# Kernel tuning notes

Measured on AMD Instinct MI355X. Metric: run time of the kernel, lower is better.

Reference implementation:

```python
import jax, jax.numpy as jnp
from jax import lax
import numpy as np
import math

DIM = 96      # channels
HEADS = 3     # num_heads
WS = 8        # window size
SHIFT = 4     # window_size // 2 (depth is odd -> shifted)
TLC = 64      # tlc_kernel
H = 264
W = 264


def _grid_idxes(h, w, k1, k2):
    # Faithful replication of the torch grids() tiling index logic (static ints).
    num_row = (h - 1) // k1 + 1
    num_col = (w - 1) // k2 + 1
    step_j = k2 if num_col == 1 else math.ceil((w - k2) / (num_col - 1) - 1e-8)
    step_i = k1 if num_row == 1 else math.ceil((h - k1) / (num_row - 1) - 1e-8)
    idxes = []
    i = 0
    last_i = False
    while i < h and not last_i:
        j = 0
        if i + k1 >= h:
            i = h - k1
            last_i = True
        last_j = False
        while j < w and not last_j:
            if j + k2 >= w:
                j = w - k2
                last_j = True
            idxes.append((i, j))
            j = j + step_j
        i = i + step_i
    return idxes


def setup_inputs() -> dict:
    key = jax.random.key(0)
    ks = jax.random.split(key, 4)
    return {
        "x": jax.random.normal(ks[0], (1, DIM, H, W), jnp.float32),
        "temperature": jnp.ones((HEADS, 1, 1), jnp.float32),
        "qkv_w": jax.random.normal(ks[1], (3 * DIM, DIM), jnp.float32) * 0.05,
        "dw_w": jax.random.normal(ks[2], (3 * DIM, 1, 3, 3), jnp.float32) * 0.1,
        "proj_w": jax.random.normal(ks[3], (DIM, DIM), jnp.float32) * 0.05,
    }


def reference(x, temperature, qkv_w, dw_w, proj_w):
    b, c, h, w = x.shape
    # depth % 2 == 1 -> cyclic shift
    x = jnp.roll(x, (-SHIFT, -SHIFT), axis=(2, 3))
    # 1x1 pointwise conv (no bias)
    qkv = jnp.einsum('oc,bchw->bohw', qkv_w, x)
    # 3x3 depthwise conv, padding 1
    qkv = lax.conv_general_dilated(
        qkv, dw_w, window_strides=(1, 1), padding=[(1, 1), (1, 1)],
        feature_group_count=3 * c, dimension_numbers=('NCHW', 'OIHW', 'NCHW'))
    # --- TLC grids: overlapping tiles (eval path, b == 1) ---
    k1, k2 = min(h, TLC), min(w, TLC)
    idxes = _grid_idxes(h, w, k1, k2)
    parts = jnp.concatenate([qkv[:, :, i:i + k1, j:j + k2] for (i, j) in idxes], axis=0)  # [T,3c,k1,k2]
    T, C3, th, tw = parts.shape
    nh, nw = th // WS, tw // WS
    # window partition: b c (h b0) (w b1) -> (b h w) c b0 b1 -> flatten spatial
    win = parts.reshape(T, C3, nh, WS, nw, WS).transpose(0, 2, 4, 1, 3, 5)
    win = win.reshape(T * nh * nw, C3, WS * WS)  # [Bw, 3c, 64]
    q, k, v = jnp.split(win, 3, axis=1)  # each [Bw, c, 64]
    ch = c // HEADS
    q = q.reshape(-1, HEADS, ch, WS * WS)
    k = k.reshape(-1, HEADS, ch, WS * WS)
    v = v.reshape(-1, HEADS, ch, WS * WS)
    # L2 normalize along token dim (F.normalize eps=1e-12)
    q = q / jnp.maximum(jnp.linalg.norm(q, axis=-1, keepdims=True), 1e-12)
    k = k / jnp.maximum(jnp.linalg.norm(k, axis=-1, keepdims=True), 1e-12)
    # channel attention: [Bw, head, ch, ch]
    attn = jax.nn.relu(jnp.einsum('bhcn,bhdn->bhcd', q, k) * temperature)
    out = jnp.einsum('bhcd,bhdn->bhcn', attn, v)  # [Bw, head, ch, 64]
    out = out.reshape(-1, c, WS, WS)
    # window merge back to tiles
    out = out.reshape(T, nh, nw, c, WS, WS).transpose(0, 3, 1, 4, 2, 5).reshape(T, c, th, tw)
    # --- TLC grids_inverse: scatter-add overlapping tiles and average ---
    preds = jnp.zeros((b, c, h, w), x.dtype)
    cnt = np.zeros((h, w), np.float32)
    for t, (i, j) in enumerate(idxes):
        preds = preds.at[0, :, i:i + k1, j:j + k2].add(out[t])
        cnt[i:i + k1, j:j + k2] += 1.0
    preds = preds / jnp.asarray(cnt)
    # 1x1 output projection
    out = jnp.einsum('oc,bchw->bohw', proj_w, preds)
    # undo cyclic shift
    return jnp.roll(out, (SHIFT, SHIFT), axis=(2, 3))
```

## Files before the change

kernel.cpp:

```cpp
#include <hip/hip_runtime.h>
#include <hip/hip_bf16.h>

#define HW_ 69696
#define W_ 264
#define H_ 264

typedef short bf16x8 __attribute__((ext_vector_type(8)));
typedef float f32x4 __attribute__((ext_vector_type(4)));

static __device__ __forceinline__ unsigned short f2b(float f) {
  __hip_bfloat16 h = __float2bfloat16(f);
  return *reinterpret_cast<unsigned short*>(&h);
}
static __device__ __forceinline__ float b2f(unsigned short u) {
  __hip_bfloat16 h;
  *reinterpret_cast<unsigned short*>(&h) = u;
  return __bfloat162float(h);
}
static __device__ __forceinline__ float lo_f(unsigned int u) {
  union { unsigned int i; float f; } c; c.i = u << 16; return c.f;
}
static __device__ __forceinline__ float hi_f(unsigned int u) {
  union { unsigned int i; float f; } c; c.i = u & 0xffff0000u; return c.f;
}

__global__ __launch_bounds__(256, 4) void k_gemm(const float* __restrict__ x,
                                                 const float* __restrict__ w,
                                                 unsigned short* __restrict__ outb) {
  __shared__ __align__(16) char smem[19968];
  unsigned short* As = (unsigned short*)smem;
  unsigned short* Cs = (unsigned short*)smem;

  const int tid = threadIdx.x;
  const int wid = tid >> 6, lane = tid & 63;
  const int quad = lane >> 4, lo = lane & 15;
  const int px0 = blockIdx.x * 64;
  const int px = px0 + wid * 16 + lo;

  const int y = px / W_, xx = px - y * W_;
  int y2 = y + 4; if (y2 >= H_) y2 -= H_;
  int x2 = xx + 4; if (x2 >= W_) x2 -= W_;
  const float* xb = x + y2 * W_ + x2;

  bf16x8 bf[3];
#pragma unroll
  for (int ks = 0; ks < 3; ++ks) {
    const float* xp = xb + (size_t)(ks * 32 + quad * 8) * HW_;
    float f[8];
#pragma unroll
    for (int i = 0; i < 8; ++i) f[i] = xp[(size_t)i * HW_];
    union { bf16x8 v; unsigned short s[8]; } u;
#pragma unroll
    for (int i = 0; i < 8; ++i) u.s[i] = f2b(f[i]);
    bf[ks] = u.v;
  }

  for (int oc = 0; oc < 3; ++oc) {
    __syncthreads();
    const float* wp = w + oc * 96 * 96;
    for (int l = tid; l < 96 * 24; l += 256) {
      int o = l / 24, c4 = (l - (l / 24) * 24) * 4;
      float4 v = *(const float4*)&wp[o * 96 + c4];
      unsigned int p0 = (unsigned int)f2b(v.x) | ((unsigned int)f2b(v.y) << 16);
      unsigned int p1 = (unsigned int)f2b(v.z) | ((unsigned int)f2b(v.w) << 16);
      *(uint2*)&As[o * 104 + c4] = make_uint2(p0, p1);
    }
    __syncthreads();

    f32x4 acc[6];
#pragma unroll
    for (int mt = 0; mt < 6; ++mt) acc[mt] = {0.f, 0.f, 0.f, 0.f};
#pragma unroll
    for (int ks = 0; ks < 3; ++ks) {
      const int kb = ks * 32 + quad * 8;
#pragma unroll
      for (int mt = 0; mt < 6; ++mt) {
        bf16x8 a = *(const bf16x8*)&As[(mt * 16 + lo) * 104 + kb];
        acc[mt] = __builtin_amdgcn_mfma_f32_16x16x32_bf16(a, bf[ks], acc[mt], 0, 0, 0);
      }
    }
    __syncthreads();

    const int pxl = wid * 16 + lo;
#pragma unroll
    for (int mt = 0; mt < 6; ++mt) {
      unsigned int p0 = (unsigned int)f2b(acc[mt][0]) | ((unsigned int)f2b(acc[mt][1]) << 16);
      unsigned int p1 = (unsigned int)f2b(acc[mt][2]) | ((unsigned int)f2b(acc[mt][3]) << 16);
      *(uint2*)&Cs[pxl * 104 + mt * 16 + quad * 4] = make_uint2(p0, p1);
    }
    __syncthreads();

    for (int i = tid; i < 64 * 12; i += 256) {
      int pxl2 = i & 63, j = i >> 6;
      *((uint4*)outb + (size_t)(oc * 12 + j) * HW_ + px0 + pxl2) =
          ((const uint4*)(Cs + pxl2 * 104))[j];
    }
  }
}

__global__ __launch_bounds__(256) void k_dw(const unsigned short* __restrict__ qkv,
                                            const float* __restrict__ dw,
                                            unsigned short* __restrict__ out) {
  __shared__ __align__(16) uint4 inS[18 * 66];
  const int tid = threadIdx.x;
  const int x0 = blockIdx.x * 64;
  const int y0 = blockIdx.y * 16;
  const int u = blockIdx.z;
  const uint4* plane = (const uint4*)qkv + (size_t)u * HW_;
  const float* wp = dw + u * 72;
  float wv[72];
#pragma unroll
  for (int i = 0; i < 72; ++i) wv[i] = wp[i];

  for (int idx = tid; idx < 18 * 66; idx += 256) {
    int rr = idx / 66, cc = idx - rr * 66;
    int gy = y0 - 1 + rr, gx = x0 - 1 + cc;
    uint4 v = make_uint4(0u, 0u, 0u, 0u);
    if ((unsigned)gy < (unsigned)H_ && (unsigned)gx < (unsigned)W_)
      v = plane[gy * W_ + gx];
    inS[idx] = v;
  }
  __syncthreads();

#pragma unroll
  for (int k = 0; k < 4; ++k) {
    const int oidx = k * 256 + tid;
    const int ro = oidx >> 6, co = oidx & 63;
    const int y = y0 + ro, x = x0 + co;
    float acc[8] = {0.f, 0.f, 0.f, 0.f, 0.f, 0.f, 0.f, 0.f};
#pragma unroll
    for (int dy = 0; dy < 3; ++dy)
#pragma unroll
      for (int dx = 0; dx < 3; ++dx) {
        uint4 v = inS[(ro + dy) * 66 + co + dx];
        float w0 = wv[0 * 9 + dy * 3 + dx], w1 = wv[1 * 9 + dy * 3 + dx];
        float w2 = wv[2 * 9 + dy * 3 + dx], w3 = wv[3 * 9 + dy * 3 + dx];
        float w4 = wv[4 * 9 + dy * 3 + dx], w5 = wv[5 * 9 + dy * 3 + dx];
        float w6 = wv[6 * 9 + dy * 3 + dx], w7 = wv[7 * 9 + dy * 3 + dx];
        acc[0] += w0 * lo_f(v.x); acc[1] += w1 * hi_f(v.x);
        acc[2] += w2 * lo_f(v.y); acc[3] += w3 * hi_f(v.y);
        acc[4] += w4 * lo_f(v.z); acc[5] += w5 * hi_f(v.z);
        acc[6] += w6 * lo_f(v.w); acc[7] += w7 * hi_f(v.w);
      }
    if (y < H_ && x < W_) {
      uint4 o;
      o.x = (unsigned int)f2b(acc[0]) | ((unsigned int)f2b(acc[1]) << 16);
      o.y = (unsigned int)f2b(acc[2]) | ((unsigned int)f2b(acc[3]) << 16);
      o.z = (unsigned int)f2b(acc[4]) | ((unsigned int)f2b(acc[5]) << 16);
      o.w = (unsigned int)f2b(acc[6]) | ((unsigned int)f2b(acc[7]) << 16);
      *((uint4*)out + (size_t)u * HW_ + y * W_ + x) = o;
    }
  }
}

#define P1 200
#define P8 1608
__global__ __launch_bounds__(192) void k_attn(const unsigned short* __restrict__ qd,
                                              const float* __restrict__ temp,
                                              unsigned short* __restrict__ tout) {
  __shared__ __align__(16) unsigned short flat[8 * P8];
  __shared__ __align__(16) unsigned short attnL[3 * 32 * 40];
  __shared__ float invn[3 * 32];
  const int tid = threadIdx.x;
  const int wi = blockIdx.x, t = blockIdx.y;
  const int i0 = (t / 5) * 50, j0 = (t % 5) * 50;
  const int wy = wi >> 3, wx = wi & 7;
  const int gy0 = i0 + wy * 8, gx0 = j0 + wx * 8;

  {
    const size_t base = (size_t)gy0 * W_ + gx0;
    for (int idx = tid; idx < 24 * 64; idx += 192) {
      int u = idx >> 6, rj = idx & 63, r = rj >> 3, j = rj & 7;
      uint4 v = ((const uint4*)qd)[(size_t)u * HW_ + base + r * W_ + j];
      ((uint4*)flat)[r * 201 + j * 25 + u] = v;
    }
  }
  __syncthreads();

  const int h = tid >> 6, lane = tid & 63;
  const int quad = lane >> 4, lo = lane & 15;
  const int cb = h * 32;

  bf16x8 qf[2][2], kf[2][2];
#pragma unroll
  for (int mt = 0; mt < 2; ++mt)
#pragma unroll
    for (int kt = 0; kt < 2; ++kt) {
      const int rbase = (kt * 4 + quad) * P8;
      const int cq = cb + mt * 16 + lo;
      const int ck = 96 + cb + mt * 16 + lo;
      bf16x8 q8, k8;
#pragma unroll
      for (int j = 0; j < 8; ++j) {
        q8[j] = (short)flat[rbase + j * P1 + cq];
        k8[j] = (short)flat[rbase + j * P1 + ck];
      }
      qf[mt][kt] = q8;
      kf[mt][kt] = k8;
    }

  f32x4 S[2][2];
#pragma unroll
  for (int mt = 0; mt < 2; ++mt)
#pragma unroll
    for (int nt = 0; nt < 2; ++nt) {
      S[mt][nt] = {0.f, 0.f, 0.f, 0.f};
#pragma unroll
      for (int kt = 0; kt < 2; ++kt)
        S[mt][nt] = __builtin_amdgcn_mfma_f32_16x16x32_bf16(qf[mt][kt], kf[nt][kt], S[mt][nt], 0, 0, 0);
    }

  float ivk[2];
#pragma unroll
  for (int mt = 0; mt < 2; ++mt) {
    float sq = 0.f, sk = 0.f;
#pragma unroll
    for (int kt = 0; kt < 2; ++kt)
#pragma unroll
      for (int j = 0; j < 8; ++j) {
        float a = b2f((unsigned short)qf[mt][kt][j]);
        float b = b2f((unsigned short)kf[mt][kt][j]);
        sq += a * a;
        sk += b * b;
      }
    sq += __shfl_xor(sq, 16);
    sq += __shfl_xor(sq, 32);
    sk += __shfl_xor(sk, 16);
    sk += __shfl_xor(sk, 32);
    if (quad == 0) invn[h * 32 + mt * 16 + lo] = 1.f / fmaxf(sqrtf(sq), 1e-12f);
    ivk[mt] = 1.f / fmaxf(sqrtf(sk), 1e-12f);
  }
  __syncthreads();

  const float ts = temp[h];
#pragma unroll
  for (int mt = 0; mt < 2; ++mt)
#pragma unroll
    for (int nt = 0; nt < 2; ++nt)
#pragma unroll
      for (int r = 0; r < 4; ++r) {
        int c = mt * 16 + quad * 4 + r;
        float v = S[mt][nt][r] * invn[h * 32 + c] * ivk[nt] * ts;
        attnL[(h * 32 + c) * 40 + nt * 16 + lo] = f2b(fmaxf(v, 0.f));
      }
  __syncthreads();

  bf16x8 af[2];
#pragma unroll
  for (int mt = 0; mt < 2; ++mt)
    af[mt] = *(const bf16x8*)&attnL[(h * 32 + mt * 16 + lo) * 40 + quad * 8];

  const int uv = 24 + h * 4 + quad;
  f32x4 O[2][4];
#pragma unroll
  for (int nt = 0; nt < 4; ++nt) {
    const int px = nt * 16 + lo;
    const size_t gpx = (size_t)(gy0 + (px >> 3)) * W_ + gx0 + (px & 7);
    uint4 vraw = ((const uint4*)qd)[(size_t)uv * HW_ + gpx];
    bf16x8 vf = *reinterpret_cast<bf16x8*>(&vraw);
#pragma unroll
    for (int mt = 0; mt < 2; ++mt) {
      f32x4 z = {0.f, 0.f, 0.f, 0.f};
      O[mt][nt] = __builtin_amdgcn_mfma_f32_16x16x32_bf16(af[mt], vf, z, 0, 0, 0);
    }
  }
  __syncthreads();

  unsigned short* Cs = flat;
#pragma unroll
  for (int mt = 0; mt < 2; ++mt)
#pragma unroll
    for (int nt = 0; nt < 4; ++nt) {
      const int px = nt * 16 + lo;
      unsigned int p0 = (unsigned int)f2b(O[mt][nt][0]) | ((unsigned int)f2b(O[mt][nt][1]) << 16);
      unsigned int p1 = (unsigned int)f2b(O[mt][nt][2]) | ((unsigned int)f2b(O[mt][nt][3]) << 16);
      *(uint2*)&Cs[px * 104 + cb + mt * 16 + quad * 4] = make_uint2(p0, p1);
    }
  __syncthreads();

  for (int idx = tid; idx < 64 * 12; idx += 192) {
    int rec = idx / 12, u = idx - (idx / 12) * 12;
    int r = rec >> 3, j = rec & 7;
    size_t g = (size_t)t * 4096 + (wy * 8 + r) * 64 + wx * 8 + j;
    ((uint4*)tout)[g * 12 + u] = ((const uint4*)(Cs + rec * 104))[u];
  }
}

__global__ __launch_bounds__(256, 4) void k_avgproj(const float* __restrict__ w,
                                                    const unsigned short* __restrict__ tout,
                                                    float* __restrict__ outf) {
  __shared__ __align__(16) unsigned short As[96 * 104];
  const int tid = threadIdx.x;
  const int wid = tid >> 6, lane = tid & 63;
  const int quad = lane >> 4, lo = lane & 15;
  const int px0 = blockIdx.x * 64;
  const int px = px0 + wid * 16 + lo;

  for (int l = tid; l < 96 * 24; l += 256) {
    int o = l / 24, c4 = (l - (l / 24) * 24) * 4;
    float4 v = *(const float4*)&w[o * 96 + c4];
    unsigned int p0 = (unsigned int)f2b(v.x) | ((unsigned int)f2b(v.y) << 16);
    unsigned int p1 = (unsigned int)f2b(v.z) | ((unsigned int)f2b(v.w) << 16);
    *(uint2*)&As[o * 104 + c4] = make_uint2(p0, p1);
  }

  const int y = px / W_, xx = px - y * W_;
  int loy = (y >= 64) ? (y - 14) / 50 : 0;
  int hiy = y / 50; if (hiy > 4) hiy = 4;
  int lox = (xx >= 64) ? (xx - 14) / 50 : 0;
  int hix = xx / 50; if (hix > 4) hix = 4;
  float a24[24];
#pragma unroll
  for (int i = 0; i < 24; ++i) a24[i] = 0.f;
  int cnt = 0;
  for (int ty = loy; ty <= hiy; ++ty)
    for (int tx = lox; tx <= hix; ++tx) {
      size_t rec = (size_t)(ty * 5 + tx) * 4096 + ((y - ty * 50) << 6) + (xx - tx * 50);
      const uint4* rp = (const uint4*)tout + rec * 12 + quad;
#pragma unroll
      for (int ks = 0; ks < 3; ++ks) {
        uint4 v = rp[ks * 4];
        a24[ks * 8 + 0] += lo_f(v.x); a24[ks * 8 + 1] += hi_f(v.x);
        a24[ks * 8 + 2] += lo_f(v.y); a24[ks * 8 + 3] += hi_f(v.y);
        a24[ks * 8 + 4] += lo_f(v.z); a24[ks * 8 + 5] += hi_f(v.z);
        a24[ks * 8 + 6] += lo_f(v.w); a24[ks * 8 + 7] += hi_f(v.w);
      }
      ++cnt;
    }
  const float inv = 1.f / (float)cnt;
  bf16x8 bf[3];
#pragma unroll
  for (int ks = 0; ks < 3; ++ks) {
    union { bf16x8 v; unsigned short s[8]; } u;
#pragma unroll
    for (int i = 0; i < 8; ++i) u.s[i] = f2b(a24[ks * 8 + i] * inv);
    bf[ks] = u.v;
  }
  __syncthreads();

  f32x4 acc[6];
#pragma unroll
  for (int mt = 0; mt < 6; ++mt) acc[mt] = {0.f, 0.f, 0.f, 0.f};
#pragma unroll
  for (int ks = 0; ks < 3; ++ks) {
    const int kb = ks * 32 + quad * 8;
#pragma unroll
    for (int mt = 0; mt < 6; ++mt) {
      bf16x8 a = *(const bf16x8*)&As[(mt * 16 + lo) * 104 + kb];
      acc[mt] = __builtin_amdgcn_mfma_f32_16x16x32_bf16(a, bf[ks], acc[mt], 0, 0, 0);
    }
  }

  {
    int y2 = y + 4; if (y2 >= H_) y2 -= H_;
    int x2 = xx + 4; if (x2 >= W_) x2 -= W_;
    int tp = y2 * W_ + x2;
#pragma unroll
    for (int mt = 0; mt < 6; ++mt) {
      int row = mt * 16 + quad * 4;
#pragma unroll
      for (int r = 0; r < 4; ++r)
        outf[(size_t)(row + r) * HW_ + tp] = acc[mt][r];
    }
  }
}

extern "C" void kernel_launch(void* const* d_in, const int* in_sizes, int n_in,
                              void* d_out, int out_size, void* d_ws, size_t ws_size,
                              hipStream_t stream) {
  (void)in_sizes; (void)n_in; (void)out_size; (void)ws_size;
  const float* x = (const float*)d_in[0];
  const float* temp = (const float*)d_in[1];
  const float* qkvw = (const float*)d_in[2];
  const float* dww = (const float*)d_in[3];
  const float* projw = (const float*)d_in[4];
  float* out = (float*)d_out;

  char* ws = (char*)d_ws;
  const size_t SZQ = (size_t)288 * HW_ * 2;
  unsigned short* qkvb = (unsigned short*)ws;
  unsigned short* tout = (unsigned short*)ws;
  unsigned short* qkvd = (unsigned short*)(ws + SZQ);

  k_gemm<<<dim3(1089), 256, 0, stream>>>(x, qkvw, qkvb);
  k_dw<<<dim3(5, 17, 36), 256, 0, stream>>>(qkvb, dww, qkvd);
  k_attn<<<dim3(64, 25), 192, 0, stream>>>(qkvd, temp, tout);
  k_avgproj<<<dim3(1089), 256, 0, stream>>>(projw, tout, out);
}
```

Baseline: 150.1 us.

## Widen GEMM and depthwise tiles, run attention with 256-thread blocks

The QKV GEMM now handles 128 pixels per block with two N-tiles per wave, so each weight conversion into LDS is reused across twice as many pixels and the grid is roughly halved. The depthwise conv tile widens from 64 to 132 columns, which cuts halo overhead and the number of blocks. The attention kernel moves to 256 threads with a fourth wave that only helps with loads and stores, guarded by an active flag. The larger tiles raise register and LDS use per block, which may lower occupancy, and the extra attention wave sits idle during the compute phases.

```diff
diff --git a/kernel.cpp b/kernel.cpp
--- a/kernel.cpp
+++ b/kernel.cpp
@@ -27,32 +27,36 @@
 __global__ __launch_bounds__(256, 4) void k_gemm(const float* __restrict__ x,
                                                  const float* __restrict__ w,
                                                  unsigned short* __restrict__ outb) {
-  __shared__ __align__(16) char smem[19968];
+  __shared__ __align__(16) char smem[26624];
   unsigned short* As = (unsigned short*)smem;
   unsigned short* Cs = (unsigned short*)smem;
 
   const int tid = threadIdx.x;
   const int wid = tid >> 6, lane = tid & 63;
   const int quad = lane >> 4, lo = lane & 15;
-  const int px0 = blockIdx.x * 64;
-  const int px = px0 + wid * 16 + lo;
-
-  const int y = px / W_, xx = px - y * W_;
-  int y2 = y + 4; if (y2 >= H_) y2 -= H_;
-  int x2 = xx + 4; if (x2 >= W_) x2 -= W_;
-  const float* xb = x + y2 * W_ + x2;
-
-  bf16x8 bf[3];
-#pragma unroll
-  for (int ks = 0; ks < 3; ++ks) {
-    const float* xp = xb + (size_t)(ks * 32 + quad * 8) * HW_;
-    float f[8];
-#pragma unroll
-    for (int i = 0; i < 8; ++i) f[i] = xp[(size_t)i * HW_];
-    union { bf16x8 v; unsigned short s[8]; } u;
-#pragma unroll
-    for (int i = 0; i < 8; ++i) u.s[i] = f2b(f[i]);
-    bf[ks] = u.v;
+  const int px0 = blockIdx.x * 128;
+
+  bf16x8 bf[2][3];
+#pragma unroll
+  for (int nt = 0; nt < 2; ++nt) {
+    const int px = px0 + wid * 32 + nt * 16 + lo;
+    if (px < HW_) {
+      const int y = px / W_, xx = px - y * W_;
+      int y2 = y + 4; if (y2 >= H_) y2 -= H_;
+      int x2 = xx + 4; if (x2 >= W_) x2 -= W_;
+      const float* xb = x + y2 * W_ + x2;
+#pragma unroll
+      for (int ks = 0; ks < 3; ++ks) {
+        const float* xp = xb + (size_t)(ks * 32 + quad * 8) * HW_;
+        union { bf16x8 v; unsigned short s[8]; } u;
+#pragma unroll
+        for (int i = 0; i < 8; ++i) u.s[i] = f2b(xp[(size_t)i * HW_]);
+        bf[nt][ks] = u.v;
+      }
+    } else {
+#pragma unroll
+      for (int ks = 0; ks < 3; ++ks) bf[nt][ks] = bf16x8{0, 0, 0, 0, 0, 0, 0, 0};
+    }
   }
 
   for (int oc = 0; oc < 3; ++oc) {
@@ -67,33 +71,41 @@
     }
     __syncthreads();
 
-    f32x4 acc[6];
-#pragma unroll
-    for (int mt = 0; mt < 6; ++mt) acc[mt] = {0.f, 0.f, 0.f, 0.f};
+    f32x4 acc[6][2];
+#pragma unroll
+    for (int mt = 0; mt < 6; ++mt)
+#pragma unroll
+      for (int nt = 0; nt < 2; ++nt) acc[mt][nt] = {0.f, 0.f, 0.f, 0.f};
 #pragma unroll
     for (int ks = 0; ks < 3; ++ks) {
       const int kb = ks * 32 + quad * 8;
 #pragma unroll
       for (int mt = 0; mt < 6; ++mt) {
         bf16x8 a = *(const bf16x8*)&As[(mt * 16 + lo) * 104 + kb];
-        acc[mt] = __builtin_amdgcn_mfma_f32_16x16x32_bf16(a, bf[ks], acc[mt], 0, 0, 0);
+#pragma unroll
+        for (int nt = 0; nt < 2; ++nt)
+          acc[mt][nt] = __builtin_amdgcn_mfma_f32_16x16x32_bf16(a, bf[nt][ks], acc[mt][nt], 0, 0, 0);
       }
     }
     __syncthreads();
 
-    const int pxl = wid * 16 + lo;
-#pragma unroll
-    for (int mt = 0; mt < 6; ++mt) {
-      unsigned int p0 = (unsigned int)f2b(acc[mt][0]) | ((unsigned int)f2b(acc[mt][1]) << 16);
-      unsigned int p1 = (unsigned int)f2b(acc[mt][2]) | ((unsigned int)f2b(acc[mt][3]) << 16);
-      *(uint2*)&Cs[pxl * 104 + mt * 16 + quad * 4] = make_uint2(p0, p1);
+#pragma unroll
+    for (int nt = 0; nt < 2; ++nt) {
+      const int pxl = wid * 32 + nt * 16 + lo;
+#pragma unroll
+      for (int mt = 0; mt < 6; ++mt) {
+        unsigned int p0 = (unsigned int)f2b(acc[mt][nt][0]) | ((unsigned int)f2b(acc[mt][nt][1]) << 16);
+        unsigned int p1 = (unsigned int)f2b(acc[mt][nt][2]) | ((unsigned int)f2b(acc[mt][nt][3]) << 16);
+        *(uint2*)&Cs[pxl * 104 + mt * 16 + quad * 4] = make_uint2(p0, p1);
+      }
     }
     __syncthreads();
 
-    for (int i = tid; i < 64 * 12; i += 256) {
-      int pxl2 = i & 63, j = i >> 6;
-      *((uint4*)outb + (size_t)(oc * 12 + j) * HW_ + px0 + pxl2) =
-          ((const uint4*)(Cs + pxl2 * 104))[j];
+    for (int i = tid; i < 128 * 12; i += 256) {
+      int pxl = i & 127, j = i >> 7;
+      if (px0 + pxl < HW_)
+        *((uint4*)outb + (size_t)(oc * 12 + j) * HW_ + px0 + pxl) =
+            ((const uint4*)(Cs + pxl * 104))[j];
     }
   }
 }
@@ -101,9 +113,9 @@
 __global__ __launch_bounds__(256) void k_dw(const unsigned short* __restrict__ qkv,
                                             const float* __restrict__ dw,
                                             unsigned short* __restrict__ out) {
-  __shared__ __align__(16) uint4 inS[18 * 66];
+  __shared__ __align__(16) uint4 inS[18 * 134];
   const int tid = threadIdx.x;
-  const int x0 = blockIdx.x * 64;
+  const int x0 = blockIdx.x * 132;
   const int y0 = blockIdx.y * 16;
   const int u = blockIdx.z;
   const uint4* plane = (const uint4*)qkv + (size_t)u * HW_;
@@ -112,8 +124,8 @@
 #pragma unroll
   for (int i = 0; i < 72; ++i) wv[i] = wp[i];
 
-  for (int idx = tid; idx < 18 * 66; idx += 256) {
-    int rr = idx / 66, cc = idx - rr * 66;
+  for (int idx = tid; idx < 18 * 134; idx += 256) {
+    int rr = idx / 134, cc = idx - rr * 134;
     int gy = y0 - 1 + rr, gx = x0 - 1 + cc;
     uint4 v = make_uint4(0u, 0u, 0u, 0u);
     if ((unsigned)gy < (unsigned)H_ && (unsigned)gx < (unsigned)W_)
@@ -122,17 +134,17 @@
   }
   __syncthreads();
 
-#pragma unroll
-  for (int k = 0; k < 4; ++k) {
+  for (int k = 0; k < 9; ++k) {
     const int oidx = k * 256 + tid;
-    const int ro = oidx >> 6, co = oidx & 63;
+    if (oidx >= 16 * 132) break;
+    const int ro = oidx / 132, co = oidx - ro * 132;
     const int y = y0 + ro, x = x0 + co;
     float acc[8] = {0.f, 0.f, 0.f, 0.f, 0.f, 0.f, 0.f, 0.f};
 #pragma unroll
     for (int dy = 0; dy < 3; ++dy)
 #pragma unroll
       for (int dx = 0; dx < 3; ++dx) {
-        uint4 v = inS[(ro + dy) * 66 + co + dx];
+        uint4 v = inS[(ro + dy) * 134 + co + dx];
         float w0 = wv[0 * 9 + dy * 3 + dx], w1 = wv[1 * 9 + dy * 3 + dx];
         float w2 = wv[2 * 9 + dy * 3 + dx], w3 = wv[3 * 9 + dy * 3 + dx];
         float w4 = wv[4 * 9 + dy * 3 + dx], w5 = wv[5 * 9 + dy * 3 + dx];
@@ -142,7 +154,7 @@
         acc[4] += w4 * lo_f(v.z); acc[5] += w5 * hi_f(v.z);
         acc[6] += w6 * lo_f(v.w); acc[7] += w7 * hi_f(v.w);
       }
-    if (y < H_ && x < W_) {
+    if (y < H_) {
       uint4 o;
       o.x = (unsigned int)f2b(acc[0]) | ((unsigned int)f2b(acc[1]) << 16);
       o.y = (unsigned int)f2b(acc[2]) | ((unsigned int)f2b(acc[3]) << 16);
@@ -155,9 +167,9 @@
 
 #define P1 200
 #define P8 1608
-__global__ __launch_bounds__(192) void k_attn(const unsigned short* __restrict__ qd,
-                                              const float* __restrict__ temp,
-                                              unsigned short* __restrict__ tout) {
+__global__ __launch_bounds__(256, 4) void k_attn(const unsigned short* __restrict__ qd,
+                                                 const float* __restrict__ temp,
+                                                 unsigned short* __restrict__ tout) {
   __shared__ __align__(16) unsigned short flat[8 * P8];
   __shared__ __align__(16) unsigned short attnL[3 * 32 * 40];
   __shared__ float invn[3 * 32];
@@ -169,7 +181,7 @@
 
   {
     const size_t base = (size_t)gy0 * W_ + gx0;
-    for (int idx = tid; idx < 24 * 64; idx += 192) {
+    for (int idx = tid; idx < 24 * 64; idx += 256) {
       int u = idx >> 6, rj = idx & 63, r = rj >> 3, j = rj & 7;
       uint4 v = ((const uint4*)qd)[(size_t)u * HW_ + base + r * W_ + j];
       ((uint4*)flat)[r * 201 + j * 25 + u] = v;
@@ -180,105 +192,114 @@
   const int h = tid >> 6, lane = tid & 63;
   const int quad = lane >> 4, lo = lane & 15;
   const int cb = h * 32;
+  const bool act = (h < 3);
 
   bf16x8 qf[2][2], kf[2][2];
-#pragma unroll
-  for (int mt = 0; mt < 2; ++mt)
-#pragma unroll
-    for (int kt = 0; kt < 2; ++kt) {
-      const int rbase = (kt * 4 + quad) * P8;
-      const int cq = cb + mt * 16 + lo;
-      const int ck = 96 + cb + mt * 16 + lo;
-      bf16x8 q8, k8;
-#pragma unroll
-      for (int j = 0; j < 8; ++j) {
-        q8[j] = (short)flat[rbase + j * P1 + cq];
-        k8[j] = (short)flat[rbase + j * P1 + ck];
-      }
-      qf[mt][kt] = q8;
-      kf[mt][kt] = k8;
-    }
-
   f32x4 S[2][2];
-#pragma unroll
-  for (int mt = 0; mt < 2; ++mt)
-#pragma unroll
-    for (int nt = 0; nt < 2; ++nt) {
-      S[mt][nt] = {0.f, 0.f, 0.f, 0.f};
+  float ivk[2];
+  if (act) {
+#pragma unroll
+    for (int mt = 0; mt < 2; ++mt)
+#pragma unroll
+      for (int kt = 0; kt < 2; ++kt) {
+        const int rbase = (kt * 4 + quad) * P8;
+        const int cq = cb + mt * 16 + lo;
+        const int ck = 96 + cb + mt * 16 + lo;
+        bf16x8 q8, k8;
+#pragma unroll
+        for (int j = 0; j < 8; ++j) {
+          q8[j] = (short)flat[rbase + j * P1 + cq];
+          k8[j] = (short)flat[rbase + j * P1 + ck];
+        }
+        qf[mt][kt] = q8;
+        kf[mt][kt] = k8;
+      }
+
+#pragma unroll
+    for (int mt = 0; mt < 2; ++mt)
+#pragma unroll
+      for (int nt = 0; nt < 2; ++nt) {
+        S[mt][nt] = {0.f, 0.f, 0.f, 0.f};
+#pragma unroll
+        for (int kt = 0; kt < 2; ++kt)
+          S[mt][nt] = __builtin_amdgcn_mfma_f32_16x16x32_bf16(qf[mt][kt], kf[nt][kt], S[mt][nt], 0, 0, 0);
+      }
+
+#pragma unroll
+    for (int mt = 0; mt < 2; ++mt) {
+      float sq = 0.f, sk = 0.f;
 #pragma unroll
       for (int kt = 0; kt < 2; ++kt)
-        S[mt][nt] = __builtin_amdgcn_mfma_f32_16x16x32_bf16(qf[mt][kt], kf[nt][kt], S[mt][nt], 0, 0, 0);
-    }
-
-  float ivk[2];
-#pragma unroll
-  for (int mt = 0; mt < 2; ++mt) {
-    float sq = 0.f, sk = 0.f;
-#pragma unroll
-    for (int kt = 0; kt < 2; ++kt)
-#pragma unroll
-      for (int j = 0; j < 8; ++j) {
-        float a = b2f((unsigned short)qf[mt][kt][j]);
-        float b = b2f((unsigned short)kf[mt][kt][j]);
-        sq += a * a;
-        sk += b * b;
-      }
-    sq += __shfl_xor(sq, 16);
-    sq += __shfl_xor(sq, 32);
-    sk += __shfl_xor(sk, 16);
-    sk += __shfl_xor(sk, 32);
-    if (quad == 0) invn[h * 32 + mt * 16 + lo] = 1.f / fmaxf(sqrtf(sq), 1e-12f);
-    ivk[mt] = 1.f / fmaxf(sqrtf(sk), 1e-12f);
-  }
-  __syncthreads();
-
-  const float ts = temp[h];
-#pragma unroll
-  for (int mt = 0; mt < 2; ++mt)
-#pragma unroll
-    for (int nt = 0; nt < 2; ++nt)
-#pragma unroll
-      for (int r = 0; r < 4; ++r) {
-        int c = mt * 16 + quad * 4 + r;
-        float v = S[mt][nt][r] * invn[h * 32 + c] * ivk[nt] * ts;
-        attnL[(h * 32 + c) * 40 + nt * 16 + lo] = f2b(fmaxf(v, 0.f));
-      }
-  __syncthreads();
-
-  bf16x8 af[2];
-#pragma unroll
-  for (int mt = 0; mt < 2; ++mt)
-    af[mt] = *(const bf16x8*)&attnL[(h * 32 + mt * 16 + lo) * 40 + quad * 8];
-
-  const int uv = 24 + h * 4 + quad;
+#pragma unroll
+        for (int j = 0; j < 8; ++j) {
+          float a = b2f((unsigned short)qf[mt][kt][j]);
+          float b = b2f((unsigned short)kf[mt][kt][j]);
+          sq += a * a;
+          sk += b * b;
+        }
+      sq += __shfl_xor(sq, 16);
+      sq += __shfl_xor(sq, 32);
+      sk += __shfl_xor(sk, 16);
+      sk += __shfl_xor(sk, 32);
+      if (quad == 0) invn[h * 32 + mt * 16 + lo] = 1.f / fmaxf(sqrtf(sq), 1e-12f);
+      ivk[mt] = 1.f / fmaxf(sqrtf(sk), 1e-12f);
+    }
+  }
+  __syncthreads();
+
+  if (act) {
+    const float ts = temp[h];
+#pragma unroll
+    for (int mt = 0; mt < 2; ++mt)
+#pragma unroll
+      for (int nt = 0; nt < 2; ++nt)
+#pragma unroll
+        for (int r = 0; r < 4; ++r) {
+          int c = mt * 16 + quad * 4 + r;
+          float v = S[mt][nt][r] * invn[h * 32 + c] * ivk[nt] * ts;
+          attnL[(h * 32 + c) * 40 + nt * 16 + lo] = f2b(fmaxf(v, 0.f));
+        }
+  }
+  __syncthreads();
+
   f32x4 O[2][4];
-#pragma unroll
-  for (int nt = 0; nt < 4; ++nt) {
-    const int px = nt * 16 + lo;
-    const size_t gpx = (size_t)(gy0 + (px >> 3)) * W_ + gx0 + (px & 7);
-    uint4 vraw = ((const uint4*)qd)[(size_t)uv * HW_ + gpx];
-    bf16x8 vf = *reinterpret_cast<bf16x8*>(&vraw);
-#pragma unroll
-    for (int mt = 0; mt < 2; ++mt) {
-      f32x4 z = {0.f, 0.f, 0.f, 0.f};
-      O[mt][nt] = __builtin_amdgcn_mfma_f32_16x16x32_bf16(af[mt], vf, z, 0, 0, 0);
-    }
-  }
-  __syncthreads();
-
-  unsigned short* Cs = flat;
-#pragma unroll
-  for (int mt = 0; mt < 2; ++mt)
+  if (act) {
+    bf16x8 af[2];
+#pragma unroll
+    for (int mt = 0; mt < 2; ++mt)
+      af[mt] = *(const bf16x8*)&attnL[(h * 32 + mt * 16 + lo) * 40 + quad * 8];
+
+    const int uv = 24 + h * 4 + quad;
 #pragma unroll
     for (int nt = 0; nt < 4; ++nt) {
       const int px = nt * 16 + lo;
-      unsigned int p0 = (unsigned int)f2b(O[mt][nt][0]) | ((unsigned int)f2b(O[mt][nt][1]) << 16);
-      unsigned int p1 = (unsigned int)f2b(O[mt][nt][2]) | ((unsigned int)f2b(O[mt][nt][3]) << 16);
-      *(uint2*)&Cs[px * 104 + cb + mt * 16 + quad * 4] = make_uint2(p0, p1);
-    }
-  __syncthreads();
-
-  for (int idx = tid; idx < 64 * 12; idx += 192) {
+      const size_t gpx = (size_t)(gy0 + (px >> 3)) * W_ + gx0 + (px & 7);
+      uint4 vraw = ((const uint4*)qd)[(size_t)uv * HW_ + gpx];
+      bf16x8 vf = *reinterpret_cast<bf16x8*>(&vraw);
+#pragma unroll
+      for (int mt = 0; mt < 2; ++mt) {
+        f32x4 z = {0.f, 0.f, 0.f, 0.f};
+        O[mt][nt] = __builtin_amdgcn_mfma_f32_16x16x32_bf16(af[mt], vf, z, 0, 0, 0);
+      }
+    }
+  }
+  __syncthreads();
+
+  unsigned short* Cs = flat;
+  if (act) {
+#pragma unroll
+    for (int mt = 0; mt < 2; ++mt)
+#pragma unroll
+      for (int nt = 0; nt < 4; ++nt) {
+        const int px = nt * 16 + lo;
+        unsigned int p0 = (unsigned int)f2b(O[mt][nt][0]) | ((unsigned int)f2b(O[mt][nt][1]) << 16);
+        unsigned int p1 = (unsigned int)f2b(O[mt][nt][2]) | ((unsigned int)f2b(O[mt][nt][3]) << 16);
+        *(uint2*)&Cs[px * 104 + cb + mt * 16 + quad * 4] = make_uint2(p0, p1);
+      }
+  }
+  __syncthreads();
+
+  for (int idx = tid; idx < 64 * 12; idx += 256) {
     int rec = idx / 12, u = idx - (idx / 12) * 12;
     int r = rec >> 3, j = rec & 7;
     size_t g = (size_t)t * 4096 + (wy * 8 + r) * 64 + wx * 8 + j;
@@ -382,8 +403,8 @@
   unsigned short* tout = (unsigned short*)ws;
   unsigned short* qkvd = (unsigned short*)(ws + SZQ);
 
-  k_gemm<<<dim3(1089), 256, 0, stream>>>(x, qkvw, qkvb);
-  k_dw<<<dim3(5, 17, 36), 256, 0, stream>>>(qkvb, dww, qkvd);
-  k_attn<<<dim3(64, 25), 192, 0, stream>>>(qkvd, temp, tout);
+  k_gemm<<<dim3(545), 256, 0, stream>>>(x, qkvw, qkvb);
+  k_dw<<<dim3(2, 17, 36), 256, 0, stream>>>(qkvb, dww, qkvd);
+  k_attn<<<dim3(64, 25), 256, 0, stream>>>(qkvd, temp, tout);
   k_avgproj<<<dim3(1089), 256, 0, stream>>>(projw, tout, out);
 }
```

After: 151.8 us. About the same (+1.2%).

## Fuse pointwise qkv GEMM with depthwise 3x3 conv using halo tiles in LDS

Applied to the files above, without the earlier changes.

Merges the 1x1 qkv GEMM and the 3x3 depthwise conv into one kernel. Each block computes the GEMM on a 22x8 tile plus a one-pixel halo (24x10) and keeps the bf16 result in shared memory, then applies the depthwise conv directly from LDS. This removes the full round trip of the intermediate qkv tensor through global memory and one kernel launch. In exchange the halo pixels are recomputed (about 240 GEMM pixels per 176 outputs), shared-memory use grows, and occupancy drops (launch bounds 256,2).

```diff
diff --git a/kernel.cpp b/kernel.cpp
--- a/kernel.cpp
+++ b/kernel.cpp
@@ -24,35 +24,50 @@
   union { unsigned int i; float f; } c; c.i = u & 0xffff0000u; return c.f;
 }
 
-__global__ __launch_bounds__(256, 4) void k_gemm(const float* __restrict__ x,
-                                                 const float* __restrict__ w,
-                                                 unsigned short* __restrict__ outb) {
-  __shared__ __align__(16) char smem[19968];
-  unsigned short* As = (unsigned short*)smem;
-  unsigned short* Cs = (unsigned short*)smem;
+__global__ __launch_bounds__(256, 2) void k_gemmdw(const float* __restrict__ x,
+                                                   const float* __restrict__ w,
+                                                   const float* __restrict__ dw,
+                                                   unsigned short* __restrict__ outd) {
+  __shared__ __align__(16) unsigned short As[96 * 104];
+  __shared__ __align__(16) uint4 qkvS[12 * 242];
+  __shared__ float dwS[288 * 9];
+  unsigned short* qkvS_s = (unsigned short*)qkvS;
 
   const int tid = threadIdx.x;
   const int wid = tid >> 6, lane = tid & 63;
   const int quad = lane >> 4, lo = lane & 15;
-  const int px0 = blockIdx.x * 64;
-  const int px = px0 + wid * 16 + lo;
-
-  const int y = px / W_, xx = px - y * W_;
-  int y2 = y + 4; if (y2 >= H_) y2 -= H_;
-  int x2 = xx + 4; if (x2 >= W_) x2 -= W_;
-  const float* xb = x + y2 * W_ + x2;
-
-  bf16x8 bf[3];
-#pragma unroll
-  for (int ks = 0; ks < 3; ++ks) {
-    const float* xp = xb + (size_t)(ks * 32 + quad * 8) * HW_;
-    float f[8];
-#pragma unroll
-    for (int i = 0; i < 8; ++i) f[i] = xp[(size_t)i * HW_];
-    union { bf16x8 v; unsigned short s[8]; } u;
-#pragma unroll
-    for (int i = 0; i < 8; ++i) u.s[i] = f2b(f[i]);
-    bf[ks] = u.v;
+  const int x0 = blockIdx.x * 22;
+  const int y0 = blockIdx.y * 8;
+
+  for (int l = tid; l < 288 * 9; l += 256) dwS[l] = dw[l];
+
+  bf16x8 bfr[4][3];
+  int hps[4];
+#pragma unroll
+  for (int i = 0; i < 4; ++i) {
+    const int n = wid + 4 * i;
+    if (n < 15) {
+      const int hp = n * 16 + lo;
+      hps[i] = hp;
+      const int hy = hp / 24, hx = hp - (hp / 24) * 24;
+      const int gy = y0 - 1 + hy, gx = x0 - 1 + hx;
+      if ((unsigned)gy < (unsigned)H_ && (unsigned)gx < (unsigned)W_) {
+        int ry = gy + 4; if (ry >= H_) ry -= H_;
+        int rx = gx + 4; if (rx >= W_) rx -= W_;
+        const float* xb = x + ry * W_ + rx;
+#pragma unroll
+        for (int ks = 0; ks < 3; ++ks) {
+          const float* xp = xb + (size_t)(ks * 32 + quad * 8) * HW_;
+          union { bf16x8 v; unsigned short s[8]; } u;
+#pragma unroll
+          for (int c = 0; c < 8; ++c) u.s[c] = f2b(xp[(size_t)c * HW_]);
+          bfr[i][ks] = u.v;
+        }
+      } else {
+#pragma unroll
+        for (int ks = 0; ks < 3; ++ks) bfr[i][ks] = bf16x8{0, 0, 0, 0, 0, 0, 0, 0};
+      }
+    }
   }
 
   for (int oc = 0; oc < 3; ++oc) {
@@ -67,88 +82,66 @@
     }
     __syncthreads();
 
-    f32x4 acc[6];
-#pragma unroll
-    for (int mt = 0; mt < 6; ++mt) acc[mt] = {0.f, 0.f, 0.f, 0.f};
-#pragma unroll
-    for (int ks = 0; ks < 3; ++ks) {
-      const int kb = ks * 32 + quad * 8;
-#pragma unroll
-      for (int mt = 0; mt < 6; ++mt) {
-        bf16x8 a = *(const bf16x8*)&As[(mt * 16 + lo) * 104 + kb];
-        acc[mt] = __builtin_amdgcn_mfma_f32_16x16x32_bf16(a, bf[ks], acc[mt], 0, 0, 0);
+    bf16x8 af[6][3];
+#pragma unroll
+    for (int mt = 0; mt < 6; ++mt)
+#pragma unroll
+      for (int ks = 0; ks < 3; ++ks)
+        af[mt][ks] = *(const bf16x8*)&As[(mt * 16 + lo) * 104 + ks * 32 + quad * 8];
+
+#pragma unroll
+    for (int i = 0; i < 4; ++i) {
+      const int n = wid + 4 * i;
+      if (n < 15) {
+        f32x4 acc[6];
+#pragma unroll
+        for (int mt = 0; mt < 6; ++mt) acc[mt] = {0.f, 0.f, 0.f, 0.f};
+#pragma unroll
+        for (int ks = 0; ks < 3; ++ks)
+#pragma unroll
+          for (int mt = 0; mt < 6; ++mt)
+            acc[mt] = __builtin_amdgcn_mfma_f32_16x16x32_bf16(af[mt][ks], bfr[i][ks], acc[mt], 0, 0, 0);
+        const int hp = hps[i];
+#pragma unroll
+        for (int mt = 0; mt < 6; ++mt) {
+          const int u = mt * 2 + (quad >> 1);
+          unsigned int p0 = (unsigned int)f2b(acc[mt][0]) | ((unsigned int)f2b(acc[mt][1]) << 16);
+          unsigned int p1 = (unsigned int)f2b(acc[mt][2]) | ((unsigned int)f2b(acc[mt][3]) << 16);
+          *(uint2*)&qkvS_s[(size_t)(u * 242 + hp) * 8 + (quad & 1) * 4] = make_uint2(p0, p1);
+        }
       }
     }
     __syncthreads();
 
-    const int pxl = wid * 16 + lo;
-#pragma unroll
-    for (int mt = 0; mt < 6; ++mt) {
-      unsigned int p0 = (unsigned int)f2b(acc[mt][0]) | ((unsigned int)f2b(acc[mt][1]) << 16);
-      unsigned int p1 = (unsigned int)f2b(acc[mt][2]) | ((unsigned int)f2b(acc[mt][3]) << 16);
-      *(uint2*)&Cs[pxl * 104 + mt * 16 + quad * 4] = make_uint2(p0, p1);
-    }
-    __syncthreads();
-
-    for (int i = tid; i < 64 * 12; i += 256) {
-      int pxl2 = i & 63, j = i >> 6;
-      *((uint4*)outb + (size_t)(oc * 12 + j) * HW_ + px0 + pxl2) =
-          ((const uint4*)(Cs + pxl2 * 104))[j];
-    }
-  }
-}
-
-__global__ __launch_bounds__(256) void k_dw(const unsigned short* __restrict__ qkv,
-                                            const float* __restrict__ dw,
-                                            unsigned short* __restrict__ out) {
-  __shared__ __align__(16) uint4 inS[18 * 66];
-  const int tid = threadIdx.x;
-  const int x0 = blockIdx.x * 64;
-  const int y0 = blockIdx.y * 16;
-  const int u = blockIdx.z;
-  const uint4* plane = (const uint4*)qkv + (size_t)u * HW_;
-  const float* wp = dw + u * 72;
-  float wv[72];
-#pragma unroll
-  for (int i = 0; i < 72; ++i) wv[i] = wp[i];
-
-  for (int idx = tid; idx < 18 * 66; idx += 256) {
-    int rr = idx / 66, cc = idx - rr * 66;
-    int gy = y0 - 1 + rr, gx = x0 - 1 + cc;
-    uint4 v = make_uint4(0u, 0u, 0u, 0u);
-    if ((unsigned)gy < (unsigned)H_ && (unsigned)gx < (unsigned)W_)
-      v = plane[gy * W_ + gx];
-    inS[idx] = v;
-  }
-  __syncthreads();
-
-#pragma unroll
-  for (int k = 0; k < 4; ++k) {
-    const int oidx = k * 256 + tid;
-    const int ro = oidx >> 6, co = oidx & 63;
-    const int y = y0 + ro, x = x0 + co;
-    float acc[8] = {0.f, 0.f, 0.f, 0.f, 0.f, 0.f, 0.f, 0.f};
-#pragma unroll
-    for (int dy = 0; dy < 3; ++dy)
-#pragma unroll
-      for (int dx = 0; dx < 3; ++dx) {
-        uint4 v = inS[(ro + dy) * 66 + co + dx];
-        float w0 = wv[0 * 9 + dy * 3 + dx], w1 = wv[1 * 9 + dy * 3 + dx];
-        float w2 = wv[2 * 9 + dy * 3 + dx], w3 = wv[3 * 9 + dy * 3 + dx];
-        float w4 = wv[4 * 9 + dy * 3 + dx], w5 = wv[5 * 9 + dy * 3 + dx];
-        float w6 = wv[6 * 9 + dy * 3 + dx], w7 = wv[7 * 9 + dy * 3 + dx];
-        acc[0] += w0 * lo_f(v.x); acc[1] += w1 * hi_f(v.x);
-        acc[2] += w2 * lo_f(v.y); acc[3] += w3 * hi_f(v.y);
-        acc[4] += w4 * lo_f(v.z); acc[5] += w5 * hi_f(v.z);
-        acc[6] += w6 * lo_f(v.w); acc[7] += w7 * hi_f(v.w);
-      }
-    if (y < H_ && x < W_) {
-      uint4 o;
-      o.x = (unsigned int)f2b(acc[0]) | ((unsigned int)f2b(acc[1]) << 16);
-      o.y = (unsigned int)f2b(acc[2]) | ((unsigned int)f2b(acc[3]) << 16);
-      o.z = (unsigned int)f2b(acc[4]) | ((unsigned int)f2b(acc[5]) << 16);
-      o.w = (unsigned int)f2b(acc[6]) | ((unsigned int)f2b(acc[7]) << 16);
-      *((uint4*)out + (size_t)u * HW_ + y * W_ + x) = o;
+    if (tid < 192) {
+      const int cuu = tid >> 4, cs = tid & 15;
+      float wv[72];
+      {
+        const int base = (oc * 12 + cuu) * 72;
+#pragma unroll
+        for (int i = 0; i < 72; ++i) wv[i] = dwS[base + i];
+      }
+      for (int p = cs; p < 176; p += 16) {
+        const int y = p / 22, xx = p - y * 22;
+        float acc[8] = {0.f, 0.f, 0.f, 0.f, 0.f, 0.f, 0.f, 0.f};
+#pragma unroll
+        for (int dy = 0; dy < 3; ++dy)
+#pragma unroll
+          for (int dx = 0; dx < 3; ++dx) {
+            uint4 v = qkvS[cuu * 242 + (y + dy) * 24 + (xx + dx)];
+            const int tp = dy * 3 + dx;
+            acc[0] += wv[0 * 9 + tp] * lo_f(v.x); acc[1] += wv[1 * 9 + tp] * hi_f(v.x);
+            acc[2] += wv[2 * 9 + tp] * lo_f(v.y); acc[3] += wv[3 * 9 + tp] * hi_f(v.y);
+            acc[4] += wv[4 * 9 + tp] * lo_f(v.z); acc[5] += wv[5 * 9 + tp] * hi_f(v.z);
+            acc[6] += wv[6 * 9 + tp] * lo_f(v.w); acc[7] += wv[7 * 9 + tp] * hi_f(v.w);
+          }
+        uint4 o;
+        o.x = (unsigned int)f2b(acc[0]) | ((unsigned int)f2b(acc[1]) << 16);
+        o.y = (unsigned int)f2b(acc[2]) | ((unsigned int)f2b(acc[3]) << 16);
+        o.z = (unsigned int)f2b(acc[4]) | ((unsigned int)f2b(acc[5]) << 16);
+        o.w = (unsigned int)f2b(acc[6]) | ((unsigned int)f2b(acc[7]) << 16);
+        *((uint4*)outd + (size_t)(oc * 12 + cuu) * HW_ + (y0 + y) * W_ + x0 + xx) = o;
+      }
     }
   }
 }
@@ -378,12 +371,10 @@
 
   char* ws = (char*)d_ws;
   const size_t SZQ = (size_t)288 * HW_ * 2;
-  unsigned short* qkvb = (unsigned short*)ws;
-  unsigned short* tout = (unsigned short*)ws;
-  unsigned short* qkvd = (unsigned short*)(ws + SZQ);
-
-  k_gemm<<<dim3(1089), 256, 0, stream>>>(x, qkvw, qkvb);
-  k_dw<<<dim3(5, 17, 36), 256, 0, stream>>>(qkvb, dww, qkvd);
+  unsigned short* qkvd = (unsigned short*)ws;
+  unsigned short* tout = (unsigned short*)(ws + SZQ);
+
+  k_gemmdw<<<dim3(12, 33), 256, 0, stream>>>(x, qkvw, dww, qkvd);
   k_attn<<<dim3(64, 25), 192, 0, stream>>>(qkvd, temp, tout);
   k_avgproj<<<dim3(1089), 256, 0, stream>>>(projw, tout, out);
 }
```

Measured after the change: 156.1 us. 4.1% more time.
